# Kernel tuning notes

Hardware: AMD Instinct MI355X
Metric: run time of the kernel (lower is better)

## Reference

```python
import jax, jax.numpy as jnp
import numpy as np

T, B, D = 64, 256, 2000
TN, E, H, A, V = 3000, 256, 256, 128, 128
PS, PE, S = 64, 64, 128
G1N, G1L, G2N, G2L = 1500, 4, 1500, 6


def setup_inputs():
    key = jax.random.key(0)
    ks = jax.random.split(key, 32)
    def nrm(k, shape, s=0.05):
        return jax.random.normal(k, shape, dtype=jnp.float32) * s
    inp = {}
    inp["X"] = jax.random.uniform(ks[0], (T, B, D), dtype=jnp.float32)
    inp["profiles"] = nrm(ks[1], (B, PS), 1.0)
    inp["ini_embd"] = nrm(ks[2], (TN, E), 1.0)
    inp["Wa_w"] = nrm(ks[3], (2 * E, A))
    inp["Wa_b"] = jnp.zeros((A,), jnp.float32)
    inp["Ua_w"] = nrm(ks[4], (A, 1))
    inp["gru_Wih"] = nrm(ks[5], (3 * H, E))
    inp["gru_Whh"] = nrm(ks[6], (3 * H, H))
    inp["gru_bih"] = jnp.zeros((3 * H,), jnp.float32)
    inp["gru_bhh"] = jnp.zeros((3 * H,), jnp.float32)
    inp["tranH_w"] = nrm(ks[7], (H + PE, E))
    inp["tranH_b"] = jnp.zeros((E,), jnp.float32)
    inp["out_w"] = nrm(ks[8], (H + V + PE, D))
    inp["out_b"] = jnp.zeros((D,), jnp.float32)
    inp["erase_w"] = nrm(ks[9], (E, V))
    inp["erase_b"] = jnp.zeros((V,), jnp.float32)
    inp["add_w"] = nrm(ks[10], (E, V))
    inp["add_b"] = jnp.zeros((V,), jnp.float32)
    inp["iniVam"] = nrm(ks[11], (S, V), 1.0)
    inp["emP_w"] = nrm(ks[12], (PS, PE))
    inp["emP_b"] = jnp.zeros((PE,), jnp.float32)
    inp["attnP_w"] = nrm(ks[13], (PE + V, PE))
    inp["attnP_b"] = jnp.zeros((PE,), jnp.float32)
    inp["KMIds"] = jax.random.randint(ks[14], (S,), 0, TN, dtype=jnp.int32)
    inp["leaves1"] = jax.random.randint(ks[15], (G1N, G1L), 0, TN, dtype=jnp.int32)
    inp["anc1"] = jax.random.randint(ks[16], (G1N, G1L), 0, TN, dtype=jnp.int32)
    inp["leaves2"] = jax.random.randint(ks[17], (G2N, G2L), 0, TN, dtype=jnp.int32)
    inp["anc2"] = jax.random.randint(ks[18], (G2N, G2L), 0, TN, dtype=jnp.int32)
    inp["mapInfo"] = jax.random.randint(ks[19], (D,), 0, G1N + G2N, dtype=jnp.int32)
    lens = jnp.sort(jax.random.randint(ks[20], (B,), 1, T + 1, dtype=jnp.int32))[::-1]
    inp["X_lengths"] = lens.at[0].set(T)
    return inp


def _forward(floats, ints):
    (X, profiles, ini_embd, Wa_w, Wa_b, Ua_w, gru_Wih, gru_Whh, gru_bih, gru_bhh,
     tranH_w, tranH_b, out_w, out_b, erase_w, erase_b, add_w, add_b, iniVam,
     emP_w, emP_b, attnP_w, attnP_b) = floats
    KMIds, leaves1, anc1, leaves2, anc2, mapInfo, X_lengths = ints

    # GRAM-style ontology attention over (leaf, ancestor) pairs, grouped by path length
    def group_embed(leaves, anc):
        le = ini_embd[leaves]                                     # [N,L,E]
        ae = ini_embd[anc]                                        # [N,L,E]
        hdn = jnp.tanh(jnp.concatenate([le, ae], axis=2) @ Wa_w + Wa_b)
        w = jax.nn.softmax(hdn @ Ua_w, axis=1)                    # [N,L,1]
        return jnp.sum(w * ae, axis=1)                            # [N,E]

    embedMat = jnp.concatenate([group_embed(leaves1, anc1),
                                group_embed(leaves2, anc2)], axis=0)[mapInfo]  # [D,E]
    Xe = jnp.einsum('tbd,de->tbe', X, embedMat)                   # [T,B,E]

    # packed-sequence GRU: frozen state / zero output beyond each sample's length
    mask = (jnp.arange(T)[:, None] < X_lengths[None, :])[..., None]  # [T,B,1]

    def gru_step(h, tup):
        x_t, m_t = tup
        gx = x_t @ gru_Wih.T + gru_bih
        gh = h @ gru_Whh.T + gru_bhh
        r = jax.nn.sigmoid(gx[:, :H] + gh[:, :H])
        z = jax.nn.sigmoid(gx[:, H:2 * H] + gh[:, H:2 * H])
        n = jnp.tanh(gx[:, 2 * H:] + r * gh[:, 2 * H:])
        h_new = (1.0 - z) * n + z * h
        h = jnp.where(m_t, h_new, h)
        return h, jnp.where(m_t, h, 0.0)

    h0 = jnp.zeros((B, H), jnp.float32)
    _, gru_out = jax.lax.scan(gru_step, h0, (Xe, mask))           # [T,B,H]

    prof = profiles @ emP_w + emP_b                               # [B,PE]
    prof_rep = jnp.broadcast_to(prof[None], (T, B, PE))
    tran = jnp.concatenate([gru_out, prof_rep], axis=2) @ tranH_w + tranH_b  # [T,B,E]
    KM = ini_embd[KMIds]                                          # [S,E]
    slot_w = jax.nn.softmax(jnp.einsum('tbe,se->tbs', tran, KM), axis=2)     # [T,B,S]

    # erase/add gates depend only on Xe -> precompute, then scan VM recurrence
    erase = jax.nn.sigmoid(Xe @ erase_w + erase_b)                # [T,B,V]
    add = jnp.tanh(Xe @ add_w + add_b)                            # [T,B,V]

    def mem_step(VM, tup):
        sw, er, ad = tup                                          # [B,S],[B,V],[B,V]
        read = jnp.einsum('bs,bsv->bv', sw, VM)
        VM = VM * (1.0 - sw[:, :, None] * er[:, None, :]) + sw[:, :, None] * ad[:, None, :]
        return VM, read

    VM0 = jnp.broadcast_to(iniVam[None], (B, S, V))
    _, read = jax.lax.scan(mem_step, VM0, (slot_w, erase, add))   # read: [T,B,V]

    attn = jax.nn.relu(jnp.concatenate([prof_rep, read], axis=2) @ attnP_w + attnP_b)
    prof2 = prof_rep * attn
    final = jnp.concatenate([gru_out, read, prof2], axis=2)       # [T,B,H+V+PE]
    # dropout is identity (eval / drop_rate=0)
    return jax.nn.softmax(final @ out_w + out_b, axis=2)          # [T,B,D]


def reference(X, profiles, ini_embd, Wa_w, Wa_b, Ua_w, gru_Wih, gru_Whh, gru_bih, gru_bhh, tranH_w, tranH_b, out_w, out_b, erase_w, erase_b, add_w, add_b, iniVam, emP_w, emP_b, attnP_w, attnP_b, KMIds, leaves1, anc1, leaves2, anc2, mapInfo, X_lengths):
    floats = (X, profiles, ini_embd, Wa_w, Wa_b, Ua_w, gru_Wih, gru_Whh, gru_bih, gru_bhh,
              tranH_w, tranH_b, out_w, out_b, erase_w, erase_b, add_w, add_b, iniVam,
              emP_w, emP_b, attnP_w, attnP_b)
    ints = (KMIds, leaves1, anc1, leaves2, anc2, mapInfo, X_lengths)
    return _forward(floats, ints)
```

## Files before the change

kernel.cpp:

```cpp
#include <hip/hip_runtime.h>
#include <hip/hip_bf16.h>
#include <cmath>

#define T_  64
#define B_  256
#define D_  2000
#define TN_ 3000
#define E_  256
#define H_  256
#define A_  128
#define V_  128
#define PS_ 64
#define PE_ 64
#define S_  128
#define G1N_ 1500
#define G1L_ 4
#define G2N_ 1500
#define G2L_ 6
#define M_  (T_ * B_)
#define KF_ (H_ + V_ + PE_)
#define NREG 24

typedef __attribute__((ext_vector_type(8))) short short8_t;
typedef __attribute__((ext_vector_type(4))) float floatx4;
typedef _Float16 __attribute__((ext_vector_type(2))) h2_t;
typedef _Float16 __attribute__((ext_vector_type(8))) h8_t;

static __device__ __forceinline__ float sigmoidf_(float x) {
    return 1.0f / (1.0f + __expf(-x));
}

static __device__ __forceinline__ void bsplit_(float v, __hip_bfloat16& hi, __hip_bfloat16& lo) {
    hi = __float2bfloat16(v);
    lo = __float2bfloat16(v - __bfloat162float(hi));
}

static __device__ __forceinline__ float dot2_(unsigned int w, unsigned int h, float acc) {
    union { unsigned int u; h2_t h; } cw, ch;
    cw.u = w; ch.u = h;
#if __has_builtin(__builtin_amdgcn_fdot2)
    return __builtin_amdgcn_fdot2(cw.h, ch.h, acc, false);
#else
    return acc + (float)cw.h[0] * (float)ch.h[0] + (float)cw.h[1] * (float)ch.h[1];
#endif
}

static __device__ __forceinline__ void gl_lds16(const void* g, void* l)
{
#if __has_builtin(__builtin_amdgcn_global_load_lds)
    __builtin_amdgcn_global_load_lds(
        (const __attribute__((address_space(1))) void*)g,
        (__attribute__((address_space(3))) void*)l, 16, 0, 0);
#else
    *(short8_t*)l = *(const short8_t*)g;
#endif
}

template<int DT>
static __device__ __forceinline__ floatx4 mfma16_(short8_t a, short8_t b, floatx4 c) {
    if constexpr (DT == 0) {
        return __builtin_amdgcn_mfma_f32_16x16x32_bf16(a, b, c, 0, 0, 0);
    } else {
        union { short8_t s; h8_t h; } ua, ub;
        ua.s = a; ub.s = b;
        return __builtin_amdgcn_mfma_f32_16x16x32_f16(ua.h, ub.h, c, 0, 0, 0);
    }
}

template<int EPI, bool ACCUM, int OUTMODE, int NPH, int DT>
__global__ __launch_bounds__(256)
void k_mgemm3(const __hip_bfloat16* __restrict__ Ahi, const __hip_bfloat16* __restrict__ Alo,
              const __hip_bfloat16* __restrict__ Bhi, const __hip_bfloat16* __restrict__ Blo,
              const float* __restrict__ bias, float* __restrict__ Cf,
              __hip_bfloat16* __restrict__ Chi, __hip_bfloat16* __restrict__ Clo,
              int K, int Nreal, int nblk)
{
    __shared__ __align__(16) short As[2][4096];
    __shared__ __align__(16) short Bs[2][4096];

    const int tid  = threadIdx.x;
    const int lane = tid & 63;
    const int w    = tid >> 6;
    const int wm   = w >> 1, wn = w & 1;
    const int lr   = lane & 15;
    const int lkc  = lane >> 4;

    const int bx = blockIdx.x;
    const int xcd = bx & 7, loc = bx >> 3;
    const int mchunk = (int)gridDim.x / (8 * nblk);
    const int m0 = (xcd * mchunk + loc / nblk) * 128;
    const int n0 = (loc % nblk) * 128;

    const int fa = 2 * w;
    const size_t aoff0 = (size_t)(m0 + fa * 16 + lr) * K + lkc * 8;
    const size_t aoff1 = aoff0 + (size_t)16 * K;
    const size_t boff0 = (size_t)(n0 + fa * 16 + lr) * K + lkc * 8;
    const size_t boff1 = boff0 + (size_t)16 * K;

    const int lA0 = (fa    ) * 512 + lane * 8;
    const int lA1 = (fa + 1) * 512 + lane * 8;

    floatx4 acc[4][4];
#pragma unroll
    for (int i = 0; i < 4; ++i)
#pragma unroll
        for (int j = 0; j < 4; ++j) acc[i][j] = floatx4{0.f, 0.f, 0.f, 0.f};

    const int KT = K >> 5;
    const int NT = NPH * KT;

    int s_ph = 0, s_k = 0;
    auto do_stage = [&](int buf) {
        const __hip_bfloat16* Ap = (s_ph == 2) ? Alo : Ahi;
        const __hip_bfloat16* Bp = (s_ph == 1) ? Blo : Bhi;
        gl_lds16(Ap + aoff0 + s_k, &As[buf][lA0]);
        gl_lds16(Ap + aoff1 + s_k, &As[buf][lA1]);
        gl_lds16(Bp + boff0 + s_k, &Bs[buf][lA0]);
        gl_lds16(Bp + boff1 + s_k, &Bs[buf][lA1]);
        s_k += 32;
        if (s_k >= K) { s_k = 0; ++s_ph; }
    };

    do_stage(0);
    __syncthreads();

#pragma unroll 1
    for (int t = 0; t < NT; ++t) {
        const int cur = t & 1;
        if (t + 1 < NT) do_stage(cur ^ 1);

        short8_t af[4], bf[4];
#pragma unroll
        for (int i = 0; i < 4; ++i)
            af[i] = *(const short8_t*)(const void*)&As[cur][(wm * 4 + i) * 512 + lane * 8];
#pragma unroll
        for (int j = 0; j < 4; ++j)
            bf[j] = *(const short8_t*)(const void*)&Bs[cur][(wn * 4 + j) * 512 + lane * 8];
#pragma unroll
        for (int i = 0; i < 4; ++i)
#pragma unroll
            for (int j = 0; j < 4; ++j)
                acc[i][j] = mfma16_<DT>(af[i], bf[j], acc[i][j]);

        __syncthreads();
    }

#pragma unroll
    for (int i = 0; i < 4; ++i) {
        const int row = m0 + wm * 64 + i * 16 + (lane >> 4) * 4;
#pragma unroll
        for (int j = 0; j < 4; ++j) {
            const int col = n0 + wn * 64 + j * 16 + (lane & 15);
            if (col < Nreal) {
                float bv = bias ? bias[col] : 0.0f;
#pragma unroll
                for (int r = 0; r < 4; ++r) {
                    float v = acc[i][j][r] + bv;
                    if (EPI == 1) v = (col < 128) ? sigmoidf_(v) : tanhf(v);
                    if (EPI == 2) {
                        if (col < 128) v = sigmoidf_(v);
                        else if (col < 256) v = tanhf(v);
                    }
                    size_t o = (size_t)(row + r) * Nreal + col;
                    if (OUTMODE == 0) {
                        if (ACCUM) v += Cf[o];
                        Cf[o] = v;
                    } else if (OUTMODE == 1) {
                        __hip_bfloat16 h, l;
                        bsplit_(v, h, l);
                        Chi[o] = h; Clo[o] = l;
                    } else {
                        ((_Float16*)Chi)[o] = (_Float16)v;
                    }
                }
            }
        }
    }
}

__global__ __launch_bounds__(256)
void k_cvtX(const float* __restrict__ X, _Float16* __restrict__ XH)
{
    int idx = blockIdx.x * blockDim.x + threadIdx.x;
    if (idx >= M_ * 256) return;
    int m = idx >> 8, d0 = (idx & 255) * 8;
    _Float16 h[8];
    if (d0 + 7 < D_) {
        float4 p = *(const float4*)(X + (size_t)m * D_ + d0);
        float4 q = *(const float4*)(X + (size_t)m * D_ + d0 + 4);
        h[0]=(_Float16)p.x; h[1]=(_Float16)p.y; h[2]=(_Float16)p.z; h[3]=(_Float16)p.w;
        h[4]=(_Float16)q.x; h[5]=(_Float16)q.y; h[6]=(_Float16)q.z; h[7]=(_Float16)q.w;
    } else {
#pragma unroll
        for (int i = 0; i < 8; ++i)
            h[i] = (d0 + i < D_) ? (_Float16)X[(size_t)m * D_ + d0 + i] : (_Float16)0.0f;
    }
    *(short8_t*)(XH + (size_t)m * 2048 + d0) = *(short8_t*)h;
}

__global__ __launch_bounds__(256)
void k_mgemmXh(const _Float16* __restrict__ XH,
               const _Float16* __restrict__ Bhi, const _Float16* __restrict__ Blo,
               __hip_bfloat16* __restrict__ Chi, __hip_bfloat16* __restrict__ Clo)
{
    const int KP = 2048, NN = 256, nblk = 2;
    __shared__ __align__(16) short Ah[2][4096];
    __shared__ __align__(16) short Bh[2][4096];
    __shared__ __align__(16) short Bl[2][4096];

    const int tid  = threadIdx.x;
    const int lane = tid & 63;
    const int w    = tid >> 6;
    const int wm   = w >> 1, wn = w & 1;
    const int lr   = lane & 15;
    const int lkc  = lane >> 4;

    const int bx = blockIdx.x;
    const int xcd = bx & 7, loc = bx >> 3;
    const int mchunk = 256 / (8 * nblk);
    const int m0 = (xcd * mchunk + loc / nblk) * 128;
    const int n0 = (loc % nblk) * 128;

    const int fa = 2 * w;
    const size_t aoff0 = (size_t)(m0 + fa * 16 + lr) * KP + lkc * 8;
    const size_t aoff1 = aoff0 + (size_t)16 * KP;
    const size_t boff0 = (size_t)(n0 + fa * 16 + lr) * KP + lkc * 8;
    const size_t boff1 = boff0 + (size_t)16 * KP;

    const int lA0 = (fa    ) * 512 + lane * 8;
    const int lA1 = (fa + 1) * 512 + lane * 8;

    floatx4 acc[4][4];
#pragma unroll
    for (int i = 0; i < 4; ++i)
#pragma unroll
        for (int j = 0; j < 4; ++j) acc[i][j] = floatx4{0.f, 0.f, 0.f, 0.f};

    int s_k = 0;
    auto do_stage = [&](int buf) {
        gl_lds16(XH  + aoff0 + s_k, &Ah[buf][lA0]);
        gl_lds16(XH  + aoff1 + s_k, &Ah[buf][lA1]);
        gl_lds16(Bhi + boff0 + s_k, &Bh[buf][lA0]);
        gl_lds16(Bhi + boff1 + s_k, &Bh[buf][lA1]);
        gl_lds16(Blo + boff0 + s_k, &Bl[buf][lA0]);
        gl_lds16(Blo + boff1 + s_k, &Bl[buf][lA1]);
        s_k += 32;
    };

    do_stage(0);
    __syncthreads();

#pragma unroll 1
    for (int t = 0; t < KP / 32; ++t) {
        const int cur = t & 1;
        if (s_k < KP) do_stage(cur ^ 1);

        short8_t af[4], bfh[4], bfl[4];
#pragma unroll
        for (int i = 0; i < 4; ++i) {
            af[i]  = *(const short8_t*)(const void*)&Ah[cur][(wm * 4 + i) * 512 + lane * 8];
            bfh[i] = *(const short8_t*)(const void*)&Bh[cur][(wn * 4 + i) * 512 + lane * 8];
        }
#pragma unroll
        for (int i = 0; i < 4; ++i)
#pragma unroll
            for (int j = 0; j < 4; ++j)
                acc[i][j] = mfma16_<1>(af[i], bfh[j], acc[i][j]);
#pragma unroll
        for (int j = 0; j < 4; ++j)
            bfl[j] = *(const short8_t*)(const void*)&Bl[cur][(wn * 4 + j) * 512 + lane * 8];
#pragma unroll
        for (int i = 0; i < 4; ++i)
#pragma unroll
            for (int j = 0; j < 4; ++j)
                acc[i][j] = mfma16_<1>(af[i], bfl[j], acc[i][j]);

        __syncthreads();
    }

#pragma unroll
    for (int i = 0; i < 4; ++i) {
        const int row = m0 + wm * 64 + i * 16 + (lane >> 4) * 4;
#pragma unroll
        for (int j = 0; j < 4; ++j) {
            const int col = n0 + wn * 64 + j * 16 + (lane & 15);
#pragma unroll
            for (int r = 0; r < 4; ++r) {
                float v = acc[i][j][r];
                size_t o = (size_t)(row + r) * NN + col;
                __hip_bfloat16 h, l;
                bsplit_(v, h, l);
                Chi[o] = h; Clo[o] = l;
            }
        }
    }
}

template<int BM, int BN, int BK, int TM, int TN>
__global__ __launch_bounds__(256)
void k_gemm(const float* __restrict__ A, const float* __restrict__ B,
            float* __restrict__ C, int M, int N, int K)
{
    __shared__ float As[BK][BM + 4];
    __shared__ float Bs[BK][BN + 4];
    const int tid = threadIdx.y * blockDim.x + threadIdx.x;
    const int m0 = blockIdx.y * BM;
    const int n0 = blockIdx.x * BN;
    float acc[TM][TN];
#pragma unroll
    for (int i = 0; i < TM; ++i)
#pragma unroll
        for (int j = 0; j < TN; ++j) acc[i][j] = 0.0f;
    for (int k0 = 0; k0 < K; k0 += BK) {
#pragma unroll
        for (int i = tid; i < BM * BK; i += 256) {
            int r = i / BK, c = i % BK;
            int m = m0 + r;
            As[c][r] = (m < M) ? A[(size_t)m * K + k0 + c] : 0.0f;
        }
#pragma unroll
        for (int i = tid; i < BK * BN; i += 256) {
            int r = i / BN, c = i % BN;
            Bs[r][c] = B[(size_t)(k0 + r) * N + n0 + c];
        }
        __syncthreads();
#pragma unroll
        for (int kk = 0; kk < BK; ++kk) {
            float a[TM], b[TN];
#pragma unroll
            for (int i = 0; i < TM; ++i) a[i] = As[kk][threadIdx.y * TM + i];
#pragma unroll
            for (int j = 0; j < TN; ++j) b[j] = Bs[kk][threadIdx.x * TN + j];
#pragma unroll
            for (int i = 0; i < TM; ++i)
#pragma unroll
                for (int j = 0; j < TN; ++j) acc[i][j] += a[i] * b[j];
        }
        __syncthreads();
    }
#pragma unroll
    for (int i = 0; i < TM; ++i) {
        int m = m0 + threadIdx.y * TM + i;
        if (m >= M) continue;
#pragma unroll
        for (int j = 0; j < TN; ++j)
            C[(size_t)m * N + n0 + threadIdx.x * TN + j] = acc[i][j];
    }
}

__global__ __launch_bounds__(256)
void k_packall(const float* __restrict__ Wa_w,
               const float* __restrict__ erase_w, const float* __restrict__ add_w,
               const float* __restrict__ Wih,
               const float* __restrict__ erase_b, const float* __restrict__ add_b,
               const float* __restrict__ bih,
               const float* __restrict__ tranH_w, const float* __restrict__ out_w,
               const float* __restrict__ ini_embd, const int* __restrict__ KMIds,
               const float* __restrict__ Whh,
               float* __restrict__ W2p,
               __hip_bfloat16* __restrict__ WGhi, __hip_bfloat16* __restrict__ WGlo,
               float* __restrict__ biasG,
               __hip_bfloat16* __restrict__ THhi, __hip_bfloat16* __restrict__ THlo,
               _Float16* __restrict__ OWf,
               __hip_bfloat16* __restrict__ KMhi, __hip_bfloat16* __restrict__ KMlo,
               unsigned int* __restrict__ Wrg, unsigned int* __restrict__ Wst)
{
    int idx = blockIdx.x * blockDim.x + threadIdx.x;
    if (idx < 65536) {
        int e = idx >> 8, j = idx & 255;
        W2p[idx] = (j < A_) ? Wa_w[(size_t)e * A_ + j]
                            : Wa_w[(size_t)(E_ + e) * A_ + (j - A_)];
        return;
    }
    idx -= 65536;
    if (idx < 262144) {
        int n = idx >> 8, k = idx & 255;
        float v;
        if (n < 128)      v = erase_w[(size_t)k * V_ + n];
        else if (n < 256) v = add_w[(size_t)k * V_ + (n - 128)];
        else              v = Wih[(size_t)(n - 256) * 256 + k];
        bsplit_(v, WGhi[idx], WGlo[idx]);
        return;
    }
    idx -= 262144;
    if (idx < 1024) {
        biasG[idx] = (idx < 128) ? erase_b[idx]
                   : (idx < 256) ? add_b[idx - 128]
                                 : bih[idx - 256];
        return;
    }
    idx -= 1024;
    if (idx < 81920) {
        int n = idx / 320, k = idx % 320;
        bsplit_(tranH_w[(size_t)k * 256 + n], THhi[idx], THlo[idx]);
        return;
    }
    idx -= 81920;
    if (idx < 917504) {
        int n = idx / 448, k = idx % 448;
        OWf[idx] = (n < D_) ? (_Float16)out_w[(size_t)k * D_ + n] : (_Float16)0.0f;
        return;
    }
    idx -= 917504;
    if (idx < 32768) {
        int s = idx >> 8, k = idx & 255;
        bsplit_(ini_embd[(size_t)KMIds[s] * E_ + k], KMhi[idx], KMlo[idx]);
        return;
    }
    idx -= 32768;
    if (idx < 98304) {
        int j = idx / 128, e2 = idx % 128;
        union { unsigned int u; h2_t h; } c;
        c.h[0] = (_Float16)Whh[(size_t)j * 256 + 2 * e2];
        c.h[1] = (_Float16)Whh[(size_t)j * 256 + 2 * e2 + 1];
        if (e2 < 4 * NREG) {
            int ch = e2 >> 2, i = e2 & 3;
            Wrg[((size_t)ch * 768 + j) * 4 + i] = c.u;
        } else {
            int ee = e2 - 4 * NREG;
            Wst[((size_t)(ee >> 2) * 768 + j) * 4 + (ee & 3)] = c.u;
        }
    }
}

__global__ void k_prof(const float* __restrict__ profiles, const float* __restrict__ emP_w,
                       const float* __restrict__ emP_b, float* __restrict__ prof)
{
    int b = blockIdx.x, j = threadIdx.x;
    float acc = emP_b[j];
    for (int k = 0; k < PS_; ++k) acc += profiles[(size_t)b * PS_ + k] * emP_w[(size_t)k * PE_ + j];
    prof[(size_t)b * PE_ + j] = acc;
}

__global__ void k_embMT_f16(const float* __restrict__ embG, const int* __restrict__ mapInfo,
                            _Float16* __restrict__ hi, _Float16* __restrict__ lo)
{
    int idx = blockIdx.x * blockDim.x + threadIdx.x;
    if (idx >= 256 * 2048) return;
    int e = idx >> 11, d = idx & 2047;
    float v = (d < D_) ? embG[(size_t)mapInfo[d] * E_ + e] : 0.0f;
    _Float16 h = (_Float16)v;
    hi[idx] = h;
    lo[idx] = (_Float16)(v - (float)h);
}

__global__ void k_group_embed(const float* __restrict__ PP, const float* __restrict__ Wa_b,
                              const float* __restrict__ Ua_w, const float* __restrict__ ini_embd,
                              const int* __restrict__ leaves1, const int* __restrict__ anc1,
                              const int* __restrict__ leaves2, const int* __restrict__ anc2,
                              float* __restrict__ embedG)
{
    int n = blockIdx.x;
    int lane = threadIdx.x;
    const int* lv; const int* ac; int L;
    if (n < G1N_) { L = G1L_; lv = leaves1 + (size_t)n * G1L_; ac = anc1 + (size_t)n * G1L_; }
    else { int n2 = n - G1N_; L = G2L_; lv = leaves2 + (size_t)n2 * G2L_; ac = anc2 + (size_t)n2 * G2L_; }

    float score[6]; int ai[6];
    for (int l = 0; l < L; ++l) {
        int li = lv[l]; int av = ac[l]; ai[l] = av;
        float s = 0.0f;
        for (int a = lane; a < A_; a += 64) {
            float hv = tanhf(PP[(size_t)li * 256 + a] + PP[(size_t)av * 256 + 128 + a] + Wa_b[a]);
            s += hv * Ua_w[a];
        }
        for (int o = 32; o; o >>= 1) s += __shfl_xor(s, o);
        score[l] = s;
    }
    float mx = -1e30f;
    for (int l = 0; l < L; ++l) mx = fmaxf(mx, score[l]);
    float w[6], sum = 0.0f;
    for (int l = 0; l < L; ++l) { w[l] = __expf(score[l] - mx); sum += w[l]; }
    float inv = 1.0f / sum;
    for (int e = lane; e < E_; e += 64) {
        float acc = 0.0f;
        for (int l = 0; l < L; ++l) acc += w[l] * inv * ini_embd[(size_t)ai[l] * E_ + e];
        embedG[(size_t)n * E_ + e] = acc;
    }
}

__global__ __launch_bounds__(768, 3)
void k_gru6(const float* __restrict__ Cg, const uint4* __restrict__ Wrg4,
            const uint4* __restrict__ Wst4, const float* __restrict__ bhh,
            const int* __restrict__ X_len, const float* __restrict__ prof,
            float* __restrict__ gruo,
            __hip_bfloat16* __restrict__ At_hi, __hip_bfloat16* __restrict__ At_lo)
{
    const int b = blockIdx.x;
    const int tid = threadIdx.x;

    __shared__ uint4 h2S[32];
    __shared__ float ghS[768];
    __shared__ float gxnS[256];

    if (tid < 128) ((unsigned int*)h2S)[tid] = 0u;

    uint4 Wr[NREG];
#pragma unroll
    for (int c = 0; c < NREG; ++c) {
        Wr[c] = Wrg4[(size_t)c * 768 + tid];
        asm volatile("" : "+v"(Wr[c].x), "+v"(Wr[c].y), "+v"(Wr[c].z), "+v"(Wr[c].w));
    }

    float hreg = 0.0f;
    const int len = X_len[b];
    const float bj = bhh[tid];

    __hip_bfloat16 phi, plo;
    if (tid >= 256 && tid < 320)
        bsplit_(prof[(size_t)b * PE_ + (tid - 256)], phi, plo);

    __syncthreads();

    for (int t = 0; t < T_; ++t) {
        float gxv = Cg[((size_t)t * B_ + b) * 1024 + 256 + tid];

        uint4 Wsv[8];
#pragma unroll
        for (int s = 0; s < 8; ++s)
            Wsv[s] = Wst4[(size_t)s * 768 + tid];

        float a0 = bj;
#pragma unroll
        for (int c = 0; c < NREG; ++c) {
            uint4 h = h2S[c];
            a0 = dot2_(Wr[c].x, h.x, a0);
            a0 = dot2_(Wr[c].y, h.y, a0);
            a0 = dot2_(Wr[c].z, h.z, a0);
            a0 = dot2_(Wr[c].w, h.w, a0);
        }
#pragma unroll
        for (int s = 0; s < 8; ++s) {
            uint4 h = h2S[NREG + s];
            a0 = dot2_(Wsv[s].x, h.x, a0);
            a0 = dot2_(Wsv[s].y, h.y, a0);
            a0 = dot2_(Wsv[s].z, h.z, a0);
            a0 = dot2_(Wsv[s].w, h.w, a0);
        }

        if (tid < 512) ghS[tid] = a0 + gxv;
        else { ghS[tid] = a0; gxnS[tid - 512] = gxv; }
        __syncthreads();

        if (tid < 256) {
            float r  = sigmoidf_(ghS[tid]);
            float z  = sigmoidf_(ghS[256 + tid]);
            float nn = tanhf(gxnS[tid] + r * ghS[512 + tid]);
            float hnew = (1.0f - z) * nn + z * hreg;
            bool msk = (t < len);
            hreg = msk ? hnew : hreg;
            float ov = msk ? hreg : 0.0f;
            size_t m = (size_t)t * B_ + b;
            gruo[m * H_ + tid] = ov;
            size_t o = m * 320 + tid;
            bsplit_(ov, At_hi[o], At_lo[o]);
            float partner = __shfl_xor(hreg, 1);
            if (!(tid & 1)) {
                union { unsigned int u; h2_t h; } p;
                p.h[0] = (_Float16)hreg;
                p.h[1] = (_Float16)partner;
                ((unsigned int*)h2S)[tid >> 1] = p.u;
            }
        } else if (tid < 320) {
            size_t o = ((size_t)t * B_ + b) * 320 + tid;
            At_hi[o] = phi;
            At_lo[o] = plo;
        }
        __syncthreads();
    }
}

__global__ __launch_bounds__(256)
void k_mem(const float* __restrict__ slotw, const float* __restrict__ Cg,
           const float* __restrict__ iniVam, float* __restrict__ readv)
{
    const int b = blockIdx.x;
    const int tid = threadIdx.x;
    const int v = tid & (V_ - 1);
    const int sh = tid >> 7;
    const int sbase = sh * 64;

    float VM[64];
#pragma unroll
    for (int i = 0; i < 64; ++i) VM[i] = iniVam[(size_t)(sbase + i) * V_ + v];

    __shared__ float swL[S_];
    __shared__ float eaL[2 * V_];
    __shared__ float part[V_];

    for (int t = 0; t < T_; ++t) {
        size_t m = (size_t)t * B_ + b;
        if (tid < S_) swL[tid] = slotw[m * S_ + tid];
        eaL[tid] = Cg[m * 1024 + tid];
        __syncthreads();

        float er = eaL[v], ad = eaL[V_ + v];
        float p0 = 0.0f, p1 = 0.0f, p2 = 0.0f, p3 = 0.0f;
#pragma unroll
        for (int i = 0; i < 16; ++i) {
            float s0 = swL[sbase + 4 * i];
            float s1 = swL[sbase + 4 * i + 1];
            float s2 = swL[sbase + 4 * i + 2];
            float s3 = swL[sbase + 4 * i + 3];
            float v0 = VM[4 * i], v1 = VM[4 * i + 1], v2 = VM[4 * i + 2], v3 = VM[4 * i + 3];
            p0 += s0 * v0; p1 += s1 * v1; p2 += s2 * v2; p3 += s3 * v3;
            VM[4 * i]     = v0 * (1.0f - s0 * er) + s0 * ad;
            VM[4 * i + 1] = v1 * (1.0f - s1 * er) + s1 * ad;
            VM[4 * i + 2] = v2 * (1.0f - s2 * er) + s2 * ad;
            VM[4 * i + 3] = v3 * (1.0f - s3 * er) + s3 * ad;
        }
        float acc = (p0 + p1) + (p2 + p3);
        if (sh == 1) part[v] = acc;
        __syncthreads();
        if (sh == 0) readv[m * V_ + v] = acc + part[v];
        __syncthreads();
    }
}

__global__ __launch_bounds__(256)
void k_build_final(const float* __restrict__ gruo, const float* __restrict__ readv,
                   const float* __restrict__ prof, const float* __restrict__ attnP_w,
                   const float* __restrict__ attnP_b, _Float16* __restrict__ F)
{
    const int m = blockIdx.x;
    const int b = m & (B_ - 1);
    const int tid = threadIdx.x;
    __shared__ float rd[V_];
    __shared__ float pf[PE_];
    if (tid < V_) rd[tid] = readv[(size_t)m * V_ + tid];
    if (tid < PE_) pf[tid] = prof[(size_t)b * PE_ + tid];
    __syncthreads();

    size_t base = (size_t)m * KF_;
    F[base + tid] = (_Float16)gruo[(size_t)m * H_ + tid];
    if (tid < V_) F[base + H_ + tid] = (_Float16)rd[tid];
    if (tid < PE_) {
        float a = attnP_b[tid];
        for (int k = 0; k < PE_; ++k) a += pf[k] * attnP_w[(size_t)k * PE_ + tid];
        for (int k = 0; k < V_; ++k) a += rd[k] * attnP_w[(size_t)(PE_ + k) * PE_ + tid];
        a = fmaxf(a, 0.0f);
        F[base + H_ + V_ + tid] = (_Float16)(pf[tid] * a);
    }
}

__global__ void k_softmax128(float* __restrict__ C)
{
    const int m = blockIdx.x;
    const size_t base = (size_t)m * S_;
    const int lane = threadIdx.x;
    float a = C[base + lane], b = C[base + 64 + lane];
    float mx = fmaxf(a, b);
    for (int o = 32; o; o >>= 1) mx = fmaxf(mx, __shfl_xor(mx, o));
    float e0 = __expf(a - mx), e1 = __expf(b - mx);
    float s = e0 + e1;
    for (int o = 32; o; o >>= 1) s += __shfl_xor(s, o);
    float inv = 1.0f / s;
    C[base + lane] = e0 * inv;
    C[base + 64 + lane] = e1 * inv;
}

__global__ __launch_bounds__(256)
void k_softmax2000(const _Float16* __restrict__ L, float* __restrict__ C)
{
    const int m = blockIdx.x;
    const size_t base = (size_t)m * D_;
    const int tid = threadIdx.x;
    const int wid = tid >> 6, lane = tid & 63;
    __shared__ float red[4], red2[4];

    float v[8];
#pragma unroll
    for (int i = 0; i < 8; ++i) {
        int d = i * 256 + tid;
        v[i] = (d < D_) ? (float)L[base + d] : -1e30f;
    }
    float mx = v[0];
#pragma unroll
    for (int i = 1; i < 8; ++i) mx = fmaxf(mx, v[i]);
    for (int o = 32; o; o >>= 1) mx = fmaxf(mx, __shfl_xor(mx, o));
    if (lane == 0) red[wid] = mx;
    __syncthreads();
    mx = fmaxf(fmaxf(red[0], red[1]), fmaxf(red[2], red[3]));

    float sum = 0.0f;
#pragma unroll
    for (int i = 0; i < 8; ++i) { v[i] = __expf(v[i] - mx); sum += v[i]; }
    for (int o = 32; o; o >>= 1) sum += __shfl_xor(sum, o);
    if (lane == 0) red2[wid] = sum;
    __syncthreads();
    sum = red2[0] + red2[1] + red2[2] + red2[3];
    float inv = 1.0f / sum;
#pragma unroll
    for (int i = 0; i < 8; ++i) {
        int d = i * 256 + tid;
        if (d < D_) C[base + d] = v[i] * inv;
    }
}

extern "C" void kernel_launch(void* const* d_in, const int* in_sizes, int n_in,
                              void* d_out, int out_size, void* d_ws, size_t ws_size,
                              hipStream_t stream)
{
    const float* X        = (const float*)d_in[0];
    const float* profiles = (const float*)d_in[1];
    const float* ini_embd = (const float*)d_in[2];
    const float* Wa_w     = (const float*)d_in[3];
    const float* Wa_b     = (const float*)d_in[4];
    const float* Ua_w     = (const float*)d_in[5];
    const float* gru_Wih  = (const float*)d_in[6];
    const float* gru_Whh  = (const float*)d_in[7];
    const float* gru_bih  = (const float*)d_in[8];
    const float* gru_bhh  = (const float*)d_in[9];
    const float* tranH_w  = (const float*)d_in[10];
    const float* tranH_b  = (const float*)d_in[11];
    const float* out_w    = (const float*)d_in[12];
    const float* out_b    = (const float*)d_in[13];
    const float* erase_w  = (const float*)d_in[14];
    const float* erase_b  = (const float*)d_in[15];
    const float* add_w    = (const float*)d_in[16];
    const float* add_b    = (const float*)d_in[17];
    const float* iniVam   = (const float*)d_in[18];
    const float* emP_w    = (const float*)d_in[19];
    const float* emP_b    = (const float*)d_in[20];
    const float* attnP_w  = (const float*)d_in[21];
    const float* attnP_b  = (const float*)d_in[22];
    const int* KMIds   = (const int*)d_in[23];
    const int* leaves1 = (const int*)d_in[24];
    const int* anc1    = (const int*)d_in[25];
    const int* leaves2 = (const int*)d_in[26];
    const int* anc2    = (const int*)d_in[27];
    const int* mapInfo = (const int*)d_in[28];
    const int* X_len   = (const int*)d_in[29];

    char* ws = (char*)d_ws;
    float* out = (float*)d_out;
    typedef __hip_bfloat16 bf16;

    const size_t R0 = 0;
    const size_t R1 = 67108864;
    const size_t R2 = 83886080;
    const size_t R3 = 100663296;
    size_t P = 121634816;
    const size_t EMBHI = P; P += 1048576;
    const size_t EMBLO = P; P += 1048576;
    const size_t OWF  = P; P += 1835008;
    const size_t WGHI = P; P += 524288;
    const size_t WGLO = P; P += 524288;
    const size_t THHI = P; P += 163840;
    const size_t THLO = P; P += 163840;
    const size_t KMHI = P; P += 65536;
    const size_t KMLO = P; P += 65536;
    const size_t WRG  = P; P += 294912;
    const size_t WST  = P; P += 98304;
    const size_t PROF = P; P += 65536;
    const size_t BIAS = P; P += 4096;
    const size_t W2O  = P; P += 262144;

    float* PP      = (float*)(ws + R0);
    float* embG    = (float*)(ws + R0 + 12288000);
    _Float16* XH   = (_Float16*)(ws + R0);
    float* Cg      = (float*)(ws + R0);
    _Float16* F16  = (_Float16*)(ws + R0);
    _Float16* LG16 = (_Float16*)(ws + 16777216);
    float* gruo    = (float*)(ws + R1);
    bf16*  Xe_hi   = (bf16*)(ws + R2);
    bf16*  Xe_lo   = (bf16*)(ws + R2 + 8388608);
    bf16*  tran_hi = (bf16*)(ws + R2);
    bf16*  tran_lo = (bf16*)(ws + R2 + 8388608);
    bf16*  At_hi   = (bf16*)(ws + R3);
    bf16*  At_lo   = (bf16*)(ws + R3 + 10485760);
    float* slotw   = (float*)(ws + R3);
    float* readv   = (float*)(ws + R3 + 10485760);
    _Float16* EMBhi = (_Float16*)(ws + EMBHI);
    _Float16* EMBlo = (_Float16*)(ws + EMBLO);
    _Float16* OWf = (_Float16*)(ws + OWF);
    bf16*  WGhi = (bf16*)(ws + WGHI); bf16* WGlo = (bf16*)(ws + WGLO);
    bf16*  THhi = (bf16*)(ws + THHI); bf16* THlo = (bf16*)(ws + THLO);
    bf16*  KMhi = (bf16*)(ws + KMHI); bf16* KMlo = (bf16*)(ws + KMLO);
    unsigned int* Wrg = (unsigned int*)(ws + WRG);
    unsigned int* Wst = (unsigned int*)(ws + WST);
    float* prof  = (float*)(ws + PROF);
    float* biasG = (float*)(ws + BIAS);
    float* W2p   = (float*)(ws + W2O);

    k_packall<<<5700, 256, 0, stream>>>(Wa_w, erase_w, add_w, gru_Wih,
        erase_b, add_b, gru_bih, tranH_w, out_w, ini_embd, KMIds, gru_Whh,
        W2p, WGhi, WGlo, biasG, THhi, THlo, OWf, KMhi, KMlo, Wrg, Wst);
    k_prof<<<B_, PE_, 0, stream>>>(profiles, emP_w, emP_b, prof);

    {
        dim3 blk(16, 16);
        dim3 grid(4, (TN_ + 63) / 64);
        k_gemm<64, 64, 16, 4, 4><<<grid, blk, 0, stream>>>(ini_embd, W2p, PP, TN_, 256, E_);
    }
    k_group_embed<<<G1N_ + G2N_, 64, 0, stream>>>(PP, Wa_b, Ua_w, ini_embd,
                                                  leaves1, anc1, leaves2, anc2, embG);
    k_embMT_f16<<<(256 * 2048) / 256, 256, 0, stream>>>(embG, mapInfo, EMBhi, EMBlo);

    k_cvtX<<<(M_ * 256) / 256, 256, 0, stream>>>(X, XH);

    k_mgemmXh<<<128 * 2, 256, 0, stream>>>(XH, EMBhi, EMBlo, Xe_hi, Xe_lo);

    k_mgemm3<2, false, 0, 3, 0><<<128 * 8, 256, 0, stream>>>(Xe_hi, Xe_lo, WGhi, WGlo,
        biasG, Cg, nullptr, nullptr, 256, 1024, 8);

    k_gru6<<<256, 768, 0, stream>>>(Cg, (const uint4*)Wrg, (const uint4*)Wst,
                                    gru_bhh, X_len, prof, gruo, At_hi, At_lo);

    k_mgemm3<0, false, 1, 3, 0><<<128 * 2, 256, 0, stream>>>(At_hi, At_lo, THhi, THlo,
        tranH_b, nullptr, tran_hi, tran_lo, 320, 256, 2);

    k_mgemm3<0, false, 0, 3, 0><<<128 * 1, 256, 0, stream>>>(tran_hi, tran_lo, KMhi, KMlo,
        nullptr, slotw, nullptr, nullptr, 256, 128, 1);

    k_softmax128<<<M_, 64, 0, stream>>>(slotw);
    k_mem<<<B_, 256, 0, stream>>>(slotw, Cg, iniVam, readv);
    k_build_final<<<M_, 256, 0, stream>>>(gruo, readv, prof, attnP_w, attnP_b, F16);

    k_mgemm3<0, false, 2, 1, 1><<<128 * 16, 256, 0, stream>>>(
        (const bf16*)F16, nullptr, (const bf16*)OWf, nullptr,
        out_b, nullptr, (bf16*)LG16, nullptr, 448, 2000, 16);

    k_softmax2000<<<M_, 256, 0, stream>>>(LG16, out);
}
```

Baseline: 673.9 us.

## Stream GRU recurrent weights per step and fuse softmax, memory, final-feature kernels

```diff
diff --git a/kernel.cpp b/kernel.cpp
--- a/kernel.cpp
+++ b/kernel.cpp
@@ -19,7 +19,6 @@
 #define G2L_ 6
 #define M_  (T_ * B_)
 #define KF_ (H_ + V_ + PE_)
-#define NREG 24
 
 typedef __attribute__((ext_vector_type(8))) short short8_t;
 typedef __attribute__((ext_vector_type(4))) float floatx4;
@@ -363,7 +362,7 @@
                __hip_bfloat16* __restrict__ THhi, __hip_bfloat16* __restrict__ THlo,
                _Float16* __restrict__ OWf,
                __hip_bfloat16* __restrict__ KMhi, __hip_bfloat16* __restrict__ KMlo,
-               unsigned int* __restrict__ Wrg, unsigned int* __restrict__ Wst)
+               unsigned int* __restrict__ W4)
 {
     int idx = blockIdx.x * blockDim.x + threadIdx.x;
     if (idx < 65536) {
@@ -413,13 +412,8 @@
         union { unsigned int u; h2_t h; } c;
         c.h[0] = (_Float16)Whh[(size_t)j * 256 + 2 * e2];
         c.h[1] = (_Float16)Whh[(size_t)j * 256 + 2 * e2 + 1];
-        if (e2 < 4 * NREG) {
-            int ch = e2 >> 2, i = e2 & 3;
-            Wrg[((size_t)ch * 768 + j) * 4 + i] = c.u;
-        } else {
-            int ee = e2 - 4 * NREG;
-            Wst[((size_t)(ee >> 2) * 768 + j) * 4 + (ee & 3)] = c.u;
-        }
+        int ch = e2 >> 2, i = e2 & 3;
+        W4[((size_t)ch * 768 + j) * 4 + i] = c.u;
     }
 }
 
@@ -479,11 +473,10 @@
     }
 }
 
-__global__ __launch_bounds__(768, 3)
-void k_gru6(const float* __restrict__ Cg, const uint4* __restrict__ Wrg4,
-            const uint4* __restrict__ Wst4, const float* __restrict__ bhh,
-            const int* __restrict__ X_len, const float* __restrict__ prof,
-            float* __restrict__ gruo,
+__global__ __launch_bounds__(768)
+void k_gru7(const float* __restrict__ Cg, const uint4* __restrict__ W4,
+            const float* __restrict__ bhh, const int* __restrict__ X_len,
+            const float* __restrict__ prof, _Float16* __restrict__ F,
             __hip_bfloat16* __restrict__ At_hi, __hip_bfloat16* __restrict__ At_lo)
 {
     const int b = blockIdx.x;
@@ -495,13 +488,6 @@
 
     if (tid < 128) ((unsigned int*)h2S)[tid] = 0u;
 
-    uint4 Wr[NREG];
-#pragma unroll
-    for (int c = 0; c < NREG; ++c) {
-        Wr[c] = Wrg4[(size_t)c * 768 + tid];
-        asm volatile("" : "+v"(Wr[c].x), "+v"(Wr[c].y), "+v"(Wr[c].z), "+v"(Wr[c].w));
-    }
-
     float hreg = 0.0f;
     const int len = X_len[b];
     const float bj = bhh[tid];
@@ -512,31 +498,37 @@
 
     __syncthreads();
 
+#define DOT8(BUF, BASE)                                                     \
+    {                                                                       \
+        _Pragma("unroll")                                                   \
+        for (int s = 0; s < 8; ++s) {                                       \
+            uint4 h = h2S[(BASE) + s];                                      \
+            a0 = dot2_(BUF[s].x, h.x, a0);                                  \
+            a0 = dot2_(BUF[s].y, h.y, a0);                                  \
+            a0 = dot2_(BUF[s].z, h.z, a0);                                  \
+            a0 = dot2_(BUF[s].w, h.w, a0);                                  \
+        }                                                                   \
+    }
+#define LOAD8(BUF, BASE)                                                    \
+    {                                                                       \
+        _Pragma("unroll")                                                   \
+        for (int s = 0; s < 8; ++s)                                         \
+            BUF[s] = W4[(size_t)((BASE) + s) * 768 + tid];                  \
+    }
+
     for (int t = 0; t < T_; ++t) {
         float gxv = Cg[((size_t)t * B_ + b) * 1024 + 256 + tid];
 
-        uint4 Wsv[8];
-#pragma unroll
-        for (int s = 0; s < 8; ++s)
-            Wsv[s] = Wst4[(size_t)s * 768 + tid];
-
+        uint4 wa[8], wb[8];
+        LOAD8(wa, 0)
         float a0 = bj;
-#pragma unroll
-        for (int c = 0; c < NREG; ++c) {
-            uint4 h = h2S[c];
-            a0 = dot2_(Wr[c].x, h.x, a0);
-            a0 = dot2_(Wr[c].y, h.y, a0);
-            a0 = dot2_(Wr[c].z, h.z, a0);
-            a0 = dot2_(Wr[c].w, h.w, a0);
-        }
-#pragma unroll
-        for (int s = 0; s < 8; ++s) {
-            uint4 h = h2S[NREG + s];
-            a0 = dot2_(Wsv[s].x, h.x, a0);
-            a0 = dot2_(Wsv[s].y, h.y, a0);
-            a0 = dot2_(Wsv[s].z, h.z, a0);
-            a0 = dot2_(Wsv[s].w, h.w, a0);
-        }
+        LOAD8(wb, 8)
+        DOT8(wa, 0)
+        LOAD8(wa, 16)
+        DOT8(wb, 8)
+        LOAD8(wb, 24)
+        DOT8(wa, 16)
+        DOT8(wb, 24)
 
         if (tid < 512) ghS[tid] = a0 + gxv;
         else { ghS[tid] = a0; gxnS[tid - 512] = gxv; }
@@ -551,7 +543,7 @@
             hreg = msk ? hnew : hreg;
             float ov = msk ? hreg : 0.0f;
             size_t m = (size_t)t * B_ + b;
-            gruo[m * H_ + tid] = ov;
+            F[m * KF_ + tid] = (_Float16)ov;
             size_t o = m * 320 + tid;
             bsplit_(ov, At_hi[o], At_lo[o]);
             float partner = __shfl_xor(hreg, 1);
@@ -568,11 +560,15 @@
         }
         __syncthreads();
     }
+#undef DOT8
+#undef LOAD8
 }
 
 __global__ __launch_bounds__(256)
-void k_mem(const float* __restrict__ slotw, const float* __restrict__ Cg,
-           const float* __restrict__ iniVam, float* __restrict__ readv)
+void k_memf(const float* __restrict__ slotw, const float* __restrict__ Cg,
+            const float* __restrict__ iniVam, const float* __restrict__ prof,
+            const float* __restrict__ attnP_w, const float* __restrict__ attnP_b,
+            _Float16* __restrict__ F)
 {
     const int b = blockIdx.x;
     const int tid = threadIdx.x;
@@ -580,18 +576,43 @@
     const int sh = tid >> 7;
     const int sbase = sh * 64;
 
-    float VM[64];
-#pragma unroll
-    for (int i = 0; i < 64; ++i) VM[i] = iniVam[(size_t)(sbase + i) * V_ + v];
-
+    __shared__ float aW[(PE_ + V_) * PE_];
     __shared__ float swL[S_];
     __shared__ float eaL[2 * V_];
     __shared__ float part[V_];
+    __shared__ float rdL[V_];
+    __shared__ float pfL[PE_];
+    __shared__ float abL[PE_];
+    __shared__ float pp[4][PE_];
+
+    for (int i = tid; i < (PE_ + V_) * PE_; i += 256) aW[i] = attnP_w[i];
+    if (tid < PE_) {
+        pfL[tid] = prof[(size_t)b * PE_ + tid];
+        abL[tid] = attnP_b[tid];
+    }
+
+    float VM[64];
+#pragma unroll
+    for (int i = 0; i < 64; ++i) VM[i] = iniVam[(size_t)(sbase + i) * V_ + v];
+    __syncthreads();
 
     for (int t = 0; t < T_; ++t) {
         size_t m = (size_t)t * B_ + b;
         if (tid < S_) swL[tid] = slotw[m * S_ + tid];
         eaL[tid] = Cg[m * 1024 + tid];
+        __syncthreads();
+
+        if (tid < 64) {
+            float a = swL[tid], bb = swL[64 + tid];
+            float mx = fmaxf(a, bb);
+            for (int o = 32; o; o >>= 1) mx = fmaxf(mx, __shfl_xor(mx, o));
+            float e0 = __expf(a - mx), e1 = __expf(bb - mx);
+            float s = e0 + e1;
+            for (int o = 32; o; o >>= 1) s += __shfl_xor(s, o);
+            float inv = 1.0f / s;
+            swL[tid] = e0 * inv;
+            swL[64 + tid] = e1 * inv;
+        }
         __syncthreads();
 
         float er = eaL[v], ad = eaL[V_ + v];
@@ -612,51 +633,33 @@
         float acc = (p0 + p1) + (p2 + p3);
         if (sh == 1) part[v] = acc;
         __syncthreads();
-        if (sh == 0) readv[m * V_ + v] = acc + part[v];
-        __syncthreads();
-    }
-}
-
-__global__ __launch_bounds__(256)
-void k_build_final(const float* __restrict__ gruo, const float* __restrict__ readv,
-                   const float* __restrict__ prof, const float* __restrict__ attnP_w,
-                   const float* __restrict__ attnP_b, _Float16* __restrict__ F)
-{
-    const int m = blockIdx.x;
-    const int b = m & (B_ - 1);
-    const int tid = threadIdx.x;
-    __shared__ float rd[V_];
-    __shared__ float pf[PE_];
-    if (tid < V_) rd[tid] = readv[(size_t)m * V_ + tid];
-    if (tid < PE_) pf[tid] = prof[(size_t)b * PE_ + tid];
-    __syncthreads();
-
-    size_t base = (size_t)m * KF_;
-    F[base + tid] = (_Float16)gruo[(size_t)m * H_ + tid];
-    if (tid < V_) F[base + H_ + tid] = (_Float16)rd[tid];
-    if (tid < PE_) {
-        float a = attnP_b[tid];
-        for (int k = 0; k < PE_; ++k) a += pf[k] * attnP_w[(size_t)k * PE_ + tid];
-        for (int k = 0; k < V_; ++k) a += rd[k] * attnP_w[(size_t)(PE_ + k) * PE_ + tid];
-        a = fmaxf(a, 0.0f);
-        F[base + H_ + V_ + tid] = (_Float16)(pf[tid] * a);
-    }
-}
-
-__global__ void k_softmax128(float* __restrict__ C)
-{
-    const int m = blockIdx.x;
-    const size_t base = (size_t)m * S_;
-    const int lane = threadIdx.x;
-    float a = C[base + lane], b = C[base + 64 + lane];
-    float mx = fmaxf(a, b);
-    for (int o = 32; o; o >>= 1) mx = fmaxf(mx, __shfl_xor(mx, o));
-    float e0 = __expf(a - mx), e1 = __expf(b - mx);
-    float s = e0 + e1;
-    for (int o = 32; o; o >>= 1) s += __shfl_xor(s, o);
-    float inv = 1.0f / s;
-    C[base + lane] = e0 * inv;
-    C[base + 64 + lane] = e1 * inv;
+        if (sh == 0) {
+            float rv = acc + part[v];
+            rdL[v] = rv;
+            F[m * KF_ + H_ + v] = (_Float16)rv;
+        }
+        __syncthreads();
+
+        {
+            const int pe = tid & 63, q = tid >> 6;
+            float s = 0.0f;
+            const int k0 = q * 48;
+#pragma unroll
+            for (int k = 0; k < 48; ++k) {
+                int kk = k0 + k;
+                float xv = (kk < PE_) ? pfL[kk] : rdL[kk - PE_];
+                s += xv * aW[kk * PE_ + pe];
+            }
+            pp[q][pe] = s;
+        }
+        __syncthreads();
+        if (tid < PE_) {
+            float a = abL[tid] + ((pp[0][tid] + pp[1][tid]) + (pp[2][tid] + pp[3][tid]));
+            a = fmaxf(a, 0.0f);
+            F[m * KF_ + H_ + V_ + tid] = (_Float16)(pfL[tid] * a);
+        }
+        __syncthreads();
+    }
 }
 
 __global__ __launch_bounds__(256)
@@ -750,8 +753,7 @@
     const size_t THLO = P; P += 163840;
     const size_t KMHI = P; P += 65536;
     const size_t KMLO = P; P += 65536;
-    const size_t WRG  = P; P += 294912;
-    const size_t WST  = P; P += 98304;
+    const size_t W4O  = P; P += 393216;
     const size_t PROF = P; P += 65536;
     const size_t BIAS = P; P += 4096;
     const size_t W2O  = P; P += 262144;
@@ -760,9 +762,8 @@
     float* embG    = (float*)(ws + R0 + 12288000);
     _Float16* XH   = (_Float16*)(ws + R0);
     float* Cg      = (float*)(ws + R0);
-    _Float16* F16  = (_Float16*)(ws + R0);
-    _Float16* LG16 = (_Float16*)(ws + 16777216);
-    float* gruo    = (float*)(ws + R1);
+    _Float16* LG16 = (_Float16*)(ws + R0);
+    _Float16* F16  = (_Float16*)(ws + R1);
     bf16*  Xe_hi   = (bf16*)(ws + R2);
     bf16*  Xe_lo   = (bf16*)(ws + R2 + 8388608);
     bf16*  tran_hi = (bf16*)(ws + R2);
@@ -770,22 +771,20 @@
     bf16*  At_hi   = (bf16*)(ws + R3);
     bf16*  At_lo   = (bf16*)(ws + R3 + 10485760);
     float* slotw   = (float*)(ws + R3);
-    float* readv   = (float*)(ws + R3 + 10485760);
     _Float16* EMBhi = (_Float16*)(ws + EMBHI);
     _Float16* EMBlo = (_Float16*)(ws + EMBLO);
     _Float16* OWf = (_Float16*)(ws + OWF);
     bf16*  WGhi = (bf16*)(ws + WGHI); bf16* WGlo = (bf16*)(ws + WGLO);
     bf16*  THhi = (bf16*)(ws + THHI); bf16* THlo = (bf16*)(ws + THLO);
     bf16*  KMhi = (bf16*)(ws + KMHI); bf16* KMlo = (bf16*)(ws + KMLO);
-    unsigned int* Wrg = (unsigned int*)(ws + WRG);
-    unsigned int* Wst = (unsigned int*)(ws + WST);
+    unsigned int* W4 = (unsigned int*)(ws + W4O);
     float* prof  = (float*)(ws + PROF);
     float* biasG = (float*)(ws + BIAS);
     float* W2p   = (float*)(ws + W2O);
 
     k_packall<<<5700, 256, 0, stream>>>(Wa_w, erase_w, add_w, gru_Wih,
         erase_b, add_b, gru_bih, tranH_w, out_w, ini_embd, KMIds, gru_Whh,
-        W2p, WGhi, WGlo, biasG, THhi, THlo, OWf, KMhi, KMlo, Wrg, Wst);
+        W2p, WGhi, WGlo, biasG, THhi, THlo, OWf, KMhi, KMlo, W4);
     k_prof<<<B_, PE_, 0, stream>>>(profiles, emP_w, emP_b, prof);
 
     {
@@ -804,8 +803,8 @@
     k_mgemm3<2, false, 0, 3, 0><<<128 * 8, 256, 0, stream>>>(Xe_hi, Xe_lo, WGhi, WGlo,
         biasG, Cg, nullptr, nullptr, 256, 1024, 8);
 
-    k_gru6<<<256, 768, 0, stream>>>(Cg, (const uint4*)Wrg, (const uint4*)Wst,
-                                    gru_bhh, X_len, prof, gruo, At_hi, At_lo);
+    k_gru7<<<256, 768, 0, stream>>>(Cg, (const uint4*)W4, gru_bhh, X_len, prof,
+                                    F16, At_hi, At_lo);
 
     k_mgemm3<0, false, 1, 3, 0><<<128 * 2, 256, 0, stream>>>(At_hi, At_lo, THhi, THlo,
         tranH_b, nullptr, tran_hi, tran_lo, 320, 256, 2);
@@ -813,9 +812,7 @@
     k_mgemm3<0, false, 0, 3, 0><<<128 * 1, 256, 0, stream>>>(tran_hi, tran_lo, KMhi, KMlo,
         nullptr, slotw, nullptr, nullptr, 256, 128, 1);
 
-    k_softmax128<<<M_, 64, 0, stream>>>(slotw);
-    k_mem<<<B_, 256, 0, stream>>>(slotw, Cg, iniVam, readv);
-    k_build_final<<<M_, 256, 0, stream>>>(gruo, readv, prof, attnP_w, attnP_b, F16);
+    k_memf<<<B_, 256, 0, stream>>>(slotw, Cg, iniVam, prof, attnP_w, attnP_b, F16);
 
     k_mgemm3<0, false, 2, 1, 1><<<128 * 16, 256, 0, stream>>>(
         (const bf16*)F16, nullptr, (const bf16*)OWf, nullptr,
```

New measurement: 693.7 us. 1.03x slower.
